# Optimization experiments

Hardware: AMD Instinct MI355X
Metric: run time of the kernel (lower is better)

The kernel has to match this reference:

```python
import jax, jax.numpy as jnp
import numpy as np

K = 9  # 3x3 kernel taps

def conv2d(x, w, b):
    # stride 1, padding 1, NCHW / OIHW
    out = jax.lax.conv_general_dilated(x, w, (1, 1), ((1, 1), (1, 1)),
                                       dimension_numbers=('NCHW', 'OIHW', 'NCHW'))
    return out + b[None, :, None, None]

def deform_conv2d(x, offset, mask, w, b):
    # torchvision modulated deformable conv, kernel 3x3, stride 1, pad 1, dilation 1
    B, C, H, W = x.shape
    off = offset.reshape(B, K, 2, H, W)  # per-tap (dy, dx)
    ii = (jnp.arange(K) // 3).astype(x.dtype) - 1.0  # kernel row offset (pad=1)
    jj = (jnp.arange(K) % 3).astype(x.dtype) - 1.0   # kernel col offset
    hh = jnp.arange(H, dtype=x.dtype)[None, None, :, None]
    ww = jnp.arange(W, dtype=x.dtype)[None, None, None, :]
    py = hh + ii[None, :, None, None] + off[:, :, 0]  # [B,K,H,W] sample rows
    px = ww + jj[None, :, None, None] + off[:, :, 1]  # [B,K,H,W] sample cols

    y0 = jnp.floor(py); x0 = jnp.floor(px)
    dy = py - y0; dx = px - x0
    y0 = y0.astype(jnp.int32); x0 = x0.astype(jnp.int32)

    xf = x.reshape(B, C, H * W)

    def gather(yi, xi):
        valid = ((yi >= 0) & (yi < H) & (xi >= 0) & (xi < W)).astype(x.dtype)
        yc = jnp.clip(yi, 0, H - 1)
        xc = jnp.clip(xi, 0, W - 1)
        idx = (yc * W + xc).reshape(B, K * H * W)
        v = jax.vmap(lambda xb, ib: xb[:, ib])(xf, idx)  # [B,C,K*H*W]
        return v.reshape(B, C, K, H, W) * valid[:, None]

    v00 = gather(y0,     x0)
    v01 = gather(y0,     x0 + 1)
    v10 = gather(y0 + 1, x0)
    v11 = gather(y0 + 1, x0 + 1)

    dy = dy[:, None]; dx = dx[:, None]  # broadcast over channel dim
    val = (v00 * (1 - dy) * (1 - dx) + v01 * (1 - dy) * dx
           + v10 * dy * (1 - dx) + v11 * dy * dx)
    val = val * mask[:, None]  # sigmoid modulation, [B,1,K,H,W]

    out = jnp.einsum('ock,bckhw->bohw', w.reshape(w.shape[0], C, K), val)
    return out + b[None, :, None, None]

def setup_inputs() -> dict:
    key = jax.random.key(0)
    k1, k2, k3 = jax.random.split(key, 3)
    x = jax.random.normal(k1, (8, 3, 512, 512), dtype=jnp.float32)
    w_off = jax.random.normal(k2, (27, 3, 3, 3), dtype=jnp.float32) * 0.05
    b_off = jnp.zeros((27,), dtype=jnp.float32)
    w_def = jax.random.normal(k3, (3, 3, 3, 3), dtype=jnp.float32) * 0.1
    b_def = jnp.zeros((3,), dtype=jnp.float32)
    return {'x': x, 'w_off': w_off, 'b_off': b_off, 'w_def': w_def, 'b_def': b_def}

def reference(x, w_off, b_off, w_def, b_def):
    ow = conv2d(x, w_off, b_off)            # [B,27,H,W]
    offset = ow[:, :18]                      # 2*9 offsets
    mask = jax.nn.sigmoid(ow[:, 18:])        # 9 modulation masks
    return deform_conv2d(x, offset, mask, w_def, b_def)
```

## Files before the change

kernel.cpp:

```cpp
#include <hip/hip_runtime.h>
#include <math.h>

typedef float f2 __attribute__((ext_vector_type(2)));
typedef float f2u __attribute__((ext_vector_type(2), aligned(4)));
typedef float f4 __attribute__((ext_vector_type(4)));

#define BN 8
#define CIN 3
#define HH 512
#define WW 512
#define KK 9
#define PATCH 27
#define TAPBLK 112

__global__ void reorder_weights(const float* __restrict__ w_off,
                                const float* __restrict__ b_off,
                                const float* __restrict__ w_def,
                                float* __restrict__ ws)
{
    for (int idx = threadIdx.x; idx < KK * TAPBLK; idx += blockDim.x) {
        const int k = idx / TAPBLK;
        const int r = idx % TAPBLK;
        float v = 0.0f;
        if (r < 56) {
            const int q = r >> 1, half = r & 1;
            if (q < PATCH) v = w_off[(2 * k + half) * PATCH + q];
        } else if (r < 84) {
            const int i = r - 56;
            if (i < PATCH) v = w_off[(18 + k) * PATCH + i];
        } else if (r < 96) {
            const int j = r - 84;
            const int c = j >> 2, o = j & 3;
            if (o < 3) v = w_def[o * PATCH + c * KK + k];
        } else if (r < 100) {
            const int e = r - 96;
            if (e == 0)      v = b_off[2 * k];
            else if (e == 1) v = b_off[2 * k + 1];
            else if (e == 2) v = b_off[18 + k];
        }
        ws[idx] = v;
    }
}

__global__ __launch_bounds__(256) void deform_fused_kernel(
    const float* __restrict__ x,
    const float* __restrict__ wsw,
    const float* __restrict__ b_def,
    float* __restrict__ out)
{
    const int w = blockIdx.x * blockDim.x + threadIdx.x;
    const int h = blockIdx.y;
    const int b = blockIdx.z;

    const size_t plane = (size_t)HH * WW;
    const float* xb = x + (size_t)b * CIN * plane;

    float patch[28];
    patch[27] = 0.0f;
    #pragma unroll
    for (int c = 0; c < CIN; ++c) {
        const float* xp = xb + c * plane;
        #pragma unroll
        for (int t = 0; t < KK; ++t) {
            const int yy = h + t / 3 - 1;
            const int xx = w + t % 3 - 1;
            const bool in = ((unsigned)yy < HH) & ((unsigned)xx < WW);
            const int yc = min(max(yy, 0), HH - 1);
            const int xc = min(max(xx, 0), WW - 1);
            patch[c * KK + t] = in ? xp[yc * WW + xc] : 0.0f;
        }
    }

    f2 acc01 = { b_def[0], b_def[1] };
    float acc2 = b_def[2];

    #pragma unroll 3
    for (int k = 0; k < KK; ++k) {
        const float* blk = wsw + k * TAPBLK;

        const f4 bias = *(const f4*)(blk + 96);
        f2 oyx = { bias.x, bias.y };
        float om = bias.z;

        #pragma unroll
        for (int j = 0; j < 14; ++j) {
            const f4 wq = *(const f4*)(blk + 4 * j);
            const float p0 = patch[2 * j];
            const float p1 = patch[2 * j + 1];
            const f2 w0 = { wq.x, wq.y };
            const f2 w1 = { wq.z, wq.w };
            const f2 pp0 = { p0, p0 };
            const f2 pp1 = { p1, p1 };
            oyx = __builtin_elementwise_fma(w0, pp0, oyx);
            oyx = __builtin_elementwise_fma(w1, pp1, oyx);
        }
        #pragma unroll
        for (int j = 0; j < 7; ++j) {
            const f4 wm4 = *(const f4*)(blk + 56 + 4 * j);
            om = fmaf(wm4.x, patch[4 * j],     om);
            om = fmaf(wm4.y, patch[4 * j + 1], om);
            om = fmaf(wm4.z, patch[4 * j + 2], om);
            om = fmaf(wm4.w, patch[4 * j + 3], om);
        }

        const float m = __builtin_amdgcn_rcpf(1.0f + __expf(-om));

        const float py = (float)h + (float)(k / 3 - 1) + oyx.x;
        const float px = (float)w + (float)(k % 3 - 1) + oyx.y;
        const float y0f = floorf(py);
        const float x0f = floorf(px);
        const float dy = py - y0f;
        const float dx = px - x0f;
        const int y0 = (int)y0f;
        const int x0 = (int)x0f;

        const f2 dxp = { 1.0f - dx, dx };
        const f2 wT = dxp * (1.0f - dy);
        const f2 wB = dxp * dy;

        const int interior = ((unsigned)y0 < (HH - 1)) & ((unsigned)x0 < (WW - 1));

        if (__all(interior)) {
            const int idx = y0 * WW + x0;
            #pragma unroll
            for (int c = 0; c < CIN; ++c) {
                const float* xp = xb + c * plane + idx;
                const f2 vT = *(const f2u*)(xp);
                const f2 vB = *(const f2u*)(xp + WW);
                f2 s = vT * wT;
                s = __builtin_elementwise_fma(vB, wB, s);
                const float val = (s.x + s.y) * m;
                const f4 wq = *(const f4*)(blk + 84 + 4 * c);
                const f2 w01 = { wq.x, wq.y };
                const f2 vv = { val, val };
                acc01 = __builtin_elementwise_fma(w01, vv, acc01);
                acc2 = fmaf(wq.z, val, acc2);
            }
        } else {
            const bool vy0 = (unsigned)y0 < HH;
            const bool vy1 = (unsigned)(y0 + 1) < HH;
            const bool vx0 = (unsigned)x0 < WW;
            const bool vx1 = (unsigned)(x0 + 1) < WW;

            const int yc0 = min(max(y0, 0), HH - 1);
            const int yc1 = min(max(y0 + 1, 0), HH - 1);
            const int xc0 = min(max(x0, 0), WW - 1);
            const int xc1 = min(max(x0 + 1, 0), WW - 1);

            #pragma unroll
            for (int c = 0; c < CIN; ++c) {
                const float* xp = xb + c * plane;
                const float v00 = (vy0 & vx0) ? xp[yc0 * WW + xc0] : 0.0f;
                const float v01 = (vy0 & vx1) ? xp[yc0 * WW + xc1] : 0.0f;
                const float v10 = (vy1 & vx0) ? xp[yc1 * WW + xc0] : 0.0f;
                const float v11 = (vy1 & vx1) ? xp[yc1 * WW + xc1] : 0.0f;

                const float val =
                    (v00 * wT.x + v01 * wT.y + v10 * wB.x + v11 * wB.y) * m;
                const f4 wq = *(const f4*)(blk + 84 + 4 * c);
                const f2 w01 = { wq.x, wq.y };
                const f2 vv = { val, val };
                acc01 = __builtin_elementwise_fma(w01, vv, acc01);
                acc2 = fmaf(wq.z, val, acc2);
            }
        }
    }

    const size_t base = (size_t)b * (CIN * plane) + (size_t)h * WW + w;
    out[base]             = acc01.x;
    out[base + plane]     = acc01.y;
    out[base + 2 * plane] = acc2;
}

extern "C" void kernel_launch(void* const* d_in, const int* in_sizes, int n_in,
                              void* d_out, int out_size, void* d_ws, size_t ws_size,
                              hipStream_t stream) {
    const float* x     = (const float*)d_in[0];
    const float* w_off = (const float*)d_in[1];
    const float* b_off = (const float*)d_in[2];
    const float* w_def = (const float*)d_in[3];
    const float* b_def = (const float*)d_in[4];
    float* out = (float*)d_out;
    float* wsw = (float*)d_ws;

    reorder_weights<<<1, 256, 0, stream>>>(w_off, b_off, w_def, wsw);

    dim3 block(256, 1, 1);
    dim3 grid(WW / 256, HH, BN);
    deform_fused_kernel<<<grid, block, 0, stream>>>(x, wsw, b_def, out);
}
```

Before: 184.2 us.

## Hoist offset conv out of tap loop and make bilinear sampling branchless

Result: slower. 191.9 us (+4.2%).

```diff
diff --git a/kernel.cpp b/kernel.cpp
--- a/kernel.cpp
+++ b/kernel.cpp
@@ -11,32 +11,33 @@
 #define WW 512
 #define KK 9
 #define PATCH 27
-#define TAPBLK 112
 
 __global__ void reorder_weights(const float* __restrict__ w_off,
                                 const float* __restrict__ b_off,
                                 const float* __restrict__ w_def,
                                 float* __restrict__ ws)
 {
-    for (int idx = threadIdx.x; idx < KK * TAPBLK; idx += blockDim.x) {
-        const int k = idx / TAPBLK;
-        const int r = idx % TAPBLK;
+    for (int idx = threadIdx.x; idx < 928; idx += blockDim.x) {
         float v = 0.0f;
-        if (r < 56) {
+        if (idx < 756) {
+            const int i = idx / 28, r = idx % 28;
             const int q = r >> 1, half = r & 1;
-            if (q < PATCH) v = w_off[(2 * k + half) * PATCH + q];
-        } else if (r < 84) {
-            const int i = r - 56;
-            if (i < PATCH) v = w_off[(18 + k) * PATCH + i];
-        } else if (r < 96) {
-            const int j = r - 84;
-            const int c = j >> 2, o = j & 3;
-            if (o < 3) v = w_def[o * PATCH + c * KK + k];
-        } else if (r < 100) {
-            const int e = r - 96;
-            if (e == 0)      v = b_off[2 * k];
-            else if (e == 1) v = b_off[2 * k + 1];
-            else if (e == 2) v = b_off[18 + k];
+            if (q < 13)      v = w_off[(2 * q + half) * PATCH + i];
+            else if (!half)  v = w_off[26 * PATCH + i];
+        } else if (idx < 900) {
+            const int t = idx - 756;
+            const int k = t / 16, r = t % 16;
+            if (r < 12) {
+                const int c = r >> 2, o = r & 3;
+                if (o < 3) v = w_def[o * PATCH + c * KK + k];
+            } else if (r == 12) v = b_off[2 * k];
+            else if (r == 13)   v = b_off[2 * k + 1];
+            else if (r == 14)   v = b_off[18 + k];
+        } else {
+            const int r = idx - 900;
+            const int q = r >> 1, half = r & 1;
+            if (q < 13)      v = b_off[2 * q + half];
+            else if (!half)  v = b_off[26];
         }
         ws[idx] = v;
     }
@@ -55,8 +56,7 @@
     const size_t plane = (size_t)HH * WW;
     const float* xb = x + (size_t)b * CIN * plane;
 
-    float patch[28];
-    patch[27] = 0.0f;
+    float patch[PATCH];
     #pragma unroll
     for (int c = 0; c < CIN; ++c) {
         const float* xp = xb + c * plane;
@@ -71,42 +71,42 @@
         }
     }
 
+    f2 ow[14];
+    #pragma unroll
+    for (int q = 0; q < 14; ++q) ow[q] = *(const f2*)(wsw + 900 + 2 * q);
+
+    #pragma unroll
+    for (int i = 0; i < PATCH; ++i) {
+        const float p = patch[i];
+        const f2 pp = { p, p };
+        const f4* row = (const f4*)(wsw + i * 28);
+        #pragma unroll
+        for (int j = 0; j < 7; ++j) {
+            const f4 wq = row[j];
+            const f2 lo = { wq.x, wq.y };
+            const f2 hi = { wq.z, wq.w };
+            ow[2 * j]     = __builtin_elementwise_fma(lo, pp, ow[2 * j]);
+            ow[2 * j + 1] = __builtin_elementwise_fma(hi, pp, ow[2 * j + 1]);
+        }
+    }
+
     f2 acc01 = { b_def[0], b_def[1] };
     float acc2 = b_def[2];
 
-    #pragma unroll 3
+    #pragma unroll
     for (int k = 0; k < KK; ++k) {
-        const float* blk = wsw + k * TAPBLK;
+        const float* blk = wsw + 756 + k * 16;
 
-        const f4 bias = *(const f4*)(blk + 96);
-        f2 oyx = { bias.x, bias.y };
-        float om = bias.z;
-
-        #pragma unroll
-        for (int j = 0; j < 14; ++j) {
-            const f4 wq = *(const f4*)(blk + 4 * j);
-            const float p0 = patch[2 * j];
-            const float p1 = patch[2 * j + 1];
-            const f2 w0 = { wq.x, wq.y };
-            const f2 w1 = { wq.z, wq.w };
-            const f2 pp0 = { p0, p0 };
-            const f2 pp1 = { p1, p1 };
-            oyx = __builtin_elementwise_fma(w0, pp0, oyx);
-            oyx = __builtin_elementwise_fma(w1, pp1, oyx);
-        }
-        #pragma unroll
-        for (int j = 0; j < 7; ++j) {
-            const f4 wm4 = *(const f4*)(blk + 56 + 4 * j);
-            om = fmaf(wm4.x, patch[4 * j],     om);
-            om = fmaf(wm4.y, patch[4 * j + 1], om);
-            om = fmaf(wm4.z, patch[4 * j + 2], om);
-            om = fmaf(wm4.w, patch[4 * j + 3], om);
-        }
+        const float oy = ow[k].x;
+        const float ox = ow[k].y;
+        const float om = (k < 8) ? ((k & 1) ? ow[9 + (k >> 1)].y
+                                            : ow[9 + (k >> 1)].x)
+                                 : ow[13].x;
 
         const float m = __builtin_amdgcn_rcpf(1.0f + __expf(-om));
 
-        const float py = (float)h + (float)(k / 3 - 1) + oyx.x;
-        const float px = (float)w + (float)(k % 3 - 1) + oyx.y;
+        const float py = (float)h + (float)(k / 3 - 1) + oy;
+        const float px = (float)w + (float)(k % 3 - 1) + ox;
         const float y0f = floorf(py);
         const float x0f = floorf(px);
         const float dy = py - y0f;
@@ -114,55 +114,40 @@
         const int y0 = (int)y0f;
         const int x0 = (int)x0f;
 
-        const f2 dxp = { 1.0f - dx, dx };
-        const f2 wT = dxp * (1.0f - dy);
-        const f2 wB = dxp * dy;
+        const int xL = min(max(x0, 0), WW - 2);
+        const float w0p = 1.0f - dx;
+        const float w1p = dx;
+        const bool P = (x0 == xL);
+        const bool Q = (x0 + 1 == xL);
+        const bool R = (x0 - 1 == xL);
+        const float wa = P ? w0p : (Q ? w1p : 0.0f);
+        const float wb = P ? w1p : (R ? w0p : 0.0f);
 
-        const int interior = ((unsigned)y0 < (HH - 1)) & ((unsigned)x0 < (WW - 1));
+        const int yc0 = min(max(y0, 0), HH - 1);
+        const int yc1 = min(max(y0 + 1, 0), HH - 1);
+        const float ady = ((unsigned)y0 < HH)       ? (1.0f - dy) * m : 0.0f;
+        const float bdy = ((unsigned)(y0 + 1) < HH) ? dy * m          : 0.0f;
 
-        if (__all(interior)) {
-            const int idx = y0 * WW + x0;
-            #pragma unroll
-            for (int c = 0; c < CIN; ++c) {
-                const float* xp = xb + c * plane + idx;
-                const f2 vT = *(const f2u*)(xp);
-                const f2 vB = *(const f2u*)(xp + WW);
-                f2 s = vT * wT;
-                s = __builtin_elementwise_fma(vB, wB, s);
-                const float val = (s.x + s.y) * m;
-                const f4 wq = *(const f4*)(blk + 84 + 4 * c);
-                const f2 w01 = { wq.x, wq.y };
-                const f2 vv = { val, val };
-                acc01 = __builtin_elementwise_fma(w01, vv, acc01);
-                acc2 = fmaf(wq.z, val, acc2);
-            }
-        } else {
-            const bool vy0 = (unsigned)y0 < HH;
-            const bool vy1 = (unsigned)(y0 + 1) < HH;
-            const bool vx0 = (unsigned)x0 < WW;
-            const bool vx1 = (unsigned)(x0 + 1) < WW;
+        const f2 wxp = { wa, wb };
+        const f2 wTe = wxp * ady;
+        const f2 wBe = wxp * bdy;
 
-            const int yc0 = min(max(y0, 0), HH - 1);
-            const int yc1 = min(max(y0 + 1, 0), HH - 1);
-            const int xc0 = min(max(x0, 0), WW - 1);
-            const int xc1 = min(max(x0 + 1, 0), WW - 1);
+        const int off0 = yc0 * WW + xL;
+        const int off1 = yc1 * WW + xL;
 
-            #pragma unroll
-            for (int c = 0; c < CIN; ++c) {
-                const float* xp = xb + c * plane;
-                const float v00 = (vy0 & vx0) ? xp[yc0 * WW + xc0] : 0.0f;
-                const float v01 = (vy0 & vx1) ? xp[yc0 * WW + xc1] : 0.0f;
-                const float v10 = (vy1 & vx0) ? xp[yc1 * WW + xc0] : 0.0f;
-                const float v11 = (vy1 & vx1) ? xp[yc1 * WW + xc1] : 0.0f;
-
-                const float val =
-                    (v00 * wT.x + v01 * wT.y + v10 * wB.x + v11 * wB.y) * m;
-                const f4 wq = *(const f4*)(blk + 84 + 4 * c);
-                const f2 w01 = { wq.x, wq.y };
-                const f2 vv = { val, val };
-                acc01 = __builtin_elementwise_fma(w01, vv, acc01);
-                acc2 = fmaf(wq.z, val, acc2);
-            }
+        #pragma unroll
+        for (int c = 0; c < CIN; ++c) {
+            const float* xp = xb + c * plane;
+            const f2 vT = *(const f2u*)(xp + off0);
+            const f2 vB = *(const f2u*)(xp + off1);
+            f2 s = vT * wTe;
+            s = __builtin_elementwise_fma(vB, wBe, s);
+            const float val = s.x + s.y;
+            const f4 wq = *(const f4*)(blk + 4 * c);
+            const f2 w01 = { wq.x, wq.y };
+            const f2 vv = { val, val };
+            acc01 = __builtin_elementwise_fma(w01, vv, acc01);
+            acc2 = fmaf(wq.z, val, acc2);
         }
     }
 
```
